# Performance work log

Hardware: AMD Instinct MI355X
Metric: run time of the kernel (lower is better)

## Reference

```python
import jax, jax.numpy as jnp
import numpy as np

N_NODES = 10000
NEG_SLOPE = 0.2
EPS = 1e-16


def gat_layer(x, W, a_src, a_dst, bias, src, dst):
    # x: [N, Fin], W: [Fin, Fout], a_src/a_dst: [Fout], bias: [Fout]
    h = x @ W                                  # [N, Fout]
    al_s = h @ a_src                           # [N]
    al_d = h @ a_dst                           # [N]
    e = jax.nn.leaky_relu(al_s[src] + al_d[dst], NEG_SLOPE)   # [E]
    # segment softmax over edges grouped by destination node
    m = jax.ops.segment_max(e, dst, num_segments=N_NODES)     # [N]
    ex = jnp.exp(e - m[dst])
    s = jax.ops.segment_sum(ex, dst, num_segments=N_NODES)    # [N]
    alpha = ex / (s[dst] + EPS)                                # [E]
    out = jax.ops.segment_sum(h[src] * alpha[:, None], dst, num_segments=N_NODES)
    return out + bias


def add_self_loops(edge_index):
    loop = jnp.arange(N_NODES, dtype=edge_index.dtype)
    return jnp.concatenate([edge_index, jnp.stack([loop, loop])], axis=1)


def setup_inputs() -> dict:
    key = jax.random.key(0)
    ks = jax.random.split(key, 12)
    F_in, F_hid, F_out = 256, 256, 256
    x = jax.random.normal(ks[0], (N_NODES, F_in), dtype=jnp.float32)
    pos_edge_index = jax.random.randint(ks[1], (2, 320000), 0, N_NODES)
    edge_index = jax.random.randint(ks[2], (2, 100000), 0, N_NODES)
    sc = lambda f: 1.0 / np.sqrt(f)
    Win_W = jax.random.normal(ks[3], (F_in, F_in), dtype=jnp.float32) * sc(F_in)
    Win_b = jnp.zeros((F_in,), dtype=jnp.float32)
    W1 = jax.random.normal(ks[4], (F_in, F_hid), dtype=jnp.float32) * sc(F_in)
    a1_src = jax.random.normal(ks[5], (F_hid,), dtype=jnp.float32) * sc(F_hid)
    a1_dst = jax.random.normal(ks[6], (F_hid,), dtype=jnp.float32) * sc(F_hid)
    b1 = jnp.zeros((F_hid,), dtype=jnp.float32)
    W2 = jax.random.normal(ks[7], (F_hid, F_out), dtype=jnp.float32) * sc(F_hid)
    a2_src = jax.random.normal(ks[8], (F_out,), dtype=jnp.float32) * sc(F_out)
    a2_dst = jax.random.normal(ks[9], (F_out,), dtype=jnp.float32) * sc(F_out)
    b2 = jnp.zeros((F_out,), dtype=jnp.float32)
    return {
        "x": x, "pos_edge_index": pos_edge_index, "edge_index": edge_index,
        "Win_W": Win_W, "Win_b": Win_b,
        "W1": W1, "a1_src": a1_src, "a1_dst": a1_dst, "b1": b1,
        "W2": W2, "a2_src": a2_src, "a2_dst": a2_dst, "b2": b2,
    }


def reference(x, pos_edge_index, edge_index, Win_W, Win_b,
              W1, a1_src, a1_dst, b1, W2, a2_src, a2_dst, b2):
    ei = add_self_loops(pos_edge_index)
    src, dst = ei[0], ei[1]
    h = x @ Win_W + Win_b                       # input_weighting Linear
    h = gat_layer(h, W1, a1_src, a1_dst, b1, src, dst)
    h = gat_layer(h, W2, a2_src, a2_dst, b2, src, dst)
    logits = jnp.sum(h[edge_index[0]] * h[edge_index[1]], axis=-1)
    return logits
```

## Files before the change

### kernel.cpp

```cpp
#include <hip/hip_runtime.h>
#include <math.h>

#define FDIM 256
#define NEG_SLOPE 0.2f

typedef _Float16 half4v __attribute__((ext_vector_type(4)));
typedef _Float16 half8v __attribute__((ext_vector_type(8)));
typedef float f32x4 __attribute__((ext_vector_type(4)));


__global__ void build_phase1(const int* __restrict__ pos_ei,
                             int* __restrict__ cnt,
                             const float* __restrict__ W0, const float* __restrict__ W1,
                             const float* __restrict__ W2,
                             _Float16* __restrict__ Wt_hi, _Float16* __restrict__ Wt_lo,
                             int E_pos, int E_tot, int nbE) {
    int b = blockIdx.x;
    int tid = threadIdx.x;
    if (b < nbE) {
        int e = b * 256 + tid;
        if (e < E_tot) {
            int d = (e < E_pos) ? pos_ei[E_pos + e] : (e - E_pos);
            atomicAdd(&cnt[d], 1);
        }
    } else {
        int idx = b - nbE;
        int n = idx & 255, mat = idx >> 8;
        const float* W = (mat == 0) ? W0 : (mat == 1) ? W1 : W2;
        int k = tid;
        float v = W[k * FDIM + n];
        _Float16 hi = (_Float16)v;
        _Float16 lo = (_Float16)(v - (float)hi);
        size_t o = (size_t)mat * FDIM * FDIM + (size_t)n * FDIM + k;
        Wt_hi[o] = hi;
        Wt_lo[o] = lo;
    }
}


__global__ __launch_bounds__(1024) void scan10k(const int* __restrict__ cnt,
                                                int* __restrict__ row_ptr,
                                                int* __restrict__ fill, int N) {
    const int CH = 10;
    __shared__ int sums[1024];
    int tid = threadIdx.x;
    int base = tid * CH;
    int vals[CH];
    int s = 0;
#pragma unroll
    for (int i = 0; i < CH; ++i) {
        int idx = base + i;
        int v = (idx < N) ? cnt[idx] : 0;
        vals[i] = s;
        s += v;
    }
    sums[tid] = s;
    __syncthreads();
    for (int off = 1; off < 1024; off <<= 1) {
        int v = (tid >= off) ? sums[tid - off] : 0;
        __syncthreads();
        sums[tid] += v;
        __syncthreads();
    }
    int toff = (tid == 0) ? 0 : sums[tid - 1];
#pragma unroll
    for (int i = 0; i < CH; ++i) {
        int idx = base + i;
        if (idx < N) {
            int rp = toff + vals[i];
            row_ptr[idx] = rp;
            fill[idx] = rp;
        }
    }
    if (tid == 0) row_ptr[N] = sums[1023];
}


__global__ void scatter_edges(const int* __restrict__ pos_ei, int* __restrict__ fill,
                              int* __restrict__ srcs, int E_pos, int E_tot) {
    int e = blockIdx.x * blockDim.x + threadIdx.x;
    if (e < E_tot) {
        int s, d;
        if (e < E_pos) { s = pos_ei[e]; d = pos_ei[E_pos + e]; }
        else           { s = e - E_pos; d = s; }
        int pos = atomicAdd(&fill[d], 1);
        srcs[pos] = s;
    }
}


template <int MODE>
__global__ __launch_bounds__(256) void gemm_mfma(
        const float* __restrict__ A32,
        const _Float16* __restrict__ A_hi, const _Float16* __restrict__ A_lo,
        const _Float16* __restrict__ Bt_hi, const _Float16* __restrict__ Bt_lo,
        const float* __restrict__ bias,
        const float* __restrict__ a_src, const float* __restrict__ a_dst,
        float* __restrict__ al_s, float* __restrict__ al_d,
        _Float16* __restrict__ C_hi, _Float16* __restrict__ C_lo,
        int M) {
    __shared__ _Float16 As_hi[64][72];
    __shared__ _Float16 As_lo[64][72];
    __shared__ _Float16 Bs_hi[64][72];
    __shared__ _Float16 Bs_lo[64][72];
    int tid = threadIdx.x;
    int lane = tid & 63, w = tid >> 6;
    int wm = w >> 1, wn = w & 1;
    int quad = lane >> 4, l16 = lane & 15;
    int mBase = blockIdx.x * 64, nBase = blockIdx.y * 64;
    f32x4 acc[2][2] = {};

    for (int k0 = 0; k0 < FDIM; k0 += 64) {
        __syncthreads();
        if (MODE == 0) {
#pragma unroll
            for (int i = 0; i < 4; ++i) {
                int f = tid + i * 256;
                int m = f >> 4, kc = (f & 15) << 2;
                int row = mBase + m;
                float4 a = make_float4(0.f, 0.f, 0.f, 0.f);
                if (row < M) a = *(const float4*)(A32 + (size_t)row * FDIM + k0 + kc);
                _Float16 hx = (_Float16)a.x, hy = (_Float16)a.y;
                _Float16 hz = (_Float16)a.z, hw = (_Float16)a.w;
                half4v hi = {hx, hy, hz, hw};
                half4v lo = {(_Float16)(a.x - (float)hx), (_Float16)(a.y - (float)hy),
                             (_Float16)(a.z - (float)hz), (_Float16)(a.w - (float)hw)};
                *(half4v*)&As_hi[m][kc] = hi;
                *(half4v*)&As_lo[m][kc] = lo;
            }
        } else {
#pragma unroll
            for (int i = 0; i < 2; ++i) {
                int g = tid + i * 256;
                int m = g >> 3, gk = (g & 7) << 3;
                int row = mBase + m;
                half8v hi, lo;
                if (row < M) {
                    size_t off = (size_t)row * FDIM + k0 + gk;
                    hi = *(const half8v*)(A_hi + off);
                    lo = *(const half8v*)(A_lo + off);
                } else {
                    _Float16 z = (_Float16)0.f;
                    hi = (half8v){z, z, z, z, z, z, z, z};
                    lo = hi;
                }
                *(half8v*)&As_hi[m][gk] = hi;
                *(half8v*)&As_lo[m][gk] = lo;
            }
        }
#pragma unroll
        for (int i = 0; i < 2; ++i) {
            int g = tid + i * 256;
            int n = g >> 3, gk = (g & 7) << 3;
            size_t off = (size_t)(nBase + n) * FDIM + k0 + gk;
            *(half8v*)&Bs_hi[n][gk] = *(const half8v*)(Bt_hi + off);
            *(half8v*)&Bs_lo[n][gk] = *(const half8v*)(Bt_lo + off);
        }
        __syncthreads();
#pragma unroll
        for (int ks = 0; ks < 2; ++ks) {
            int kcol = ks * 32 + quad * 8;
            half8v aHi[2], aLo[2], bHi[2], bLo[2];
#pragma unroll
            for (int mt = 0; mt < 2; ++mt) {
                int r = wm * 32 + mt * 16 + l16;
                aHi[mt] = *(const half8v*)&As_hi[r][kcol];
                aLo[mt] = *(const half8v*)&As_lo[r][kcol];
            }
#pragma unroll
            for (int nt = 0; nt < 2; ++nt) {
                int c = wn * 32 + nt * 16 + l16;
                bHi[nt] = *(const half8v*)&Bs_hi[c][kcol];
                bLo[nt] = *(const half8v*)&Bs_lo[c][kcol];
            }
#pragma unroll
            for (int mt = 0; mt < 2; ++mt)
#pragma unroll
                for (int nt = 0; nt < 2; ++nt) {
                    acc[mt][nt] = __builtin_amdgcn_mfma_f32_16x16x32_f16(
                        aHi[mt], bHi[nt], acc[mt][nt], 0, 0, 0);
                    acc[mt][nt] = __builtin_amdgcn_mfma_f32_16x16x32_f16(
                        aHi[mt], bLo[nt], acc[mt][nt], 0, 0, 0);
                    acc[mt][nt] = __builtin_amdgcn_mfma_f32_16x16x32_f16(
                        aLo[mt], bHi[nt], acc[mt][nt], 0, 0, 0);
                }
        }
    }

    int col0 = nBase + wn * 32 + l16;
    int col1 = col0 + 16;
    if (MODE == 0) {
        float b0 = bias[col0], b1v = bias[col1];
#pragma unroll
        for (int mt = 0; mt < 2; ++mt) {
#pragma unroll
            for (int r = 0; r < 4; ++r) {
                int row = mBase + wm * 32 + mt * 16 + quad * 4 + r;
                if (row >= M) continue;
                float o0 = acc[mt][0][r] + b0;
                float o1 = acc[mt][1][r] + b1v;
                _Float16 h0 = (_Float16)o0, h1 = (_Float16)o1;
                size_t p0 = (size_t)row * FDIM + col0;
                size_t p1 = (size_t)row * FDIM + col1;
                C_hi[p0] = h0;              C_hi[p1] = h1;
                C_lo[p0] = (_Float16)(o0 - (float)h0);
                C_lo[p1] = (_Float16)(o1 - (float)h1);
            }
        }
    } else {
        float as0 = a_src[col0], as1 = a_src[col1];
        float ad0 = a_dst[col0], ad1 = a_dst[col1];
#pragma unroll
        for (int mt = 0; mt < 2; ++mt) {
#pragma unroll
            for (int r = 0; r < 4; ++r) {
                int row = mBase + wm * 32 + mt * 16 + quad * 4 + r;
                if (row < M) {
                    C_hi[(size_t)row * FDIM + col0] = (_Float16)acc[mt][0][r];
                    C_hi[(size_t)row * FDIM + col1] = (_Float16)acc[mt][1][r];
                }
                float ps = acc[mt][0][r] * as0 + acc[mt][1][r] * as1;
                float pd = acc[mt][0][r] * ad0 + acc[mt][1][r] * ad1;
#pragma unroll
                for (int off = 8; off; off >>= 1) {
                    ps += __shfl_xor(ps, off);
                    pd += __shfl_xor(pd, off);
                }
                if (l16 == 0 && row < M) {
                    atomicAdd(&al_s[row], ps);
                    atomicAdd(&al_d[row], pd);
                }
            }
        }
    }
}


__global__ __launch_bounds__(256) void softagg(
        const _Float16* __restrict__ t, const float* __restrict__ al_s,
        const float* __restrict__ al_d, const int* __restrict__ row_ptr,
        const int* __restrict__ srcs, const float* __restrict__ bias,
        _Float16* __restrict__ out_hi, _Float16* __restrict__ out_lo,
        float* __restrict__ out32, int N) {
    int wave = threadIdx.x >> 6, lane = threadIdx.x & 63;
    int node = blockIdx.x * 4 + wave;
    if (node >= N) return;
    int beg = row_ptr[node], end = row_ptr[node + 1];
    int deg = end - beg;
    float ad = al_d[node];
    const _Float16* tb = t + (size_t)lane * 4;
    float4 acc = make_float4(0.f, 0.f, 0.f, 0.f);
    float ssum = 0.f;

    if (deg <= 256) {
        float e[4];
        int sj[4];
#pragma unroll
        for (int c = 0; c < 4; ++c) {
            e[c] = -INFINITY;
            sj[c] = 0;
            int j = beg + c * 64 + lane;
            if (j < end) {
                int s = srcs[j];
                sj[c] = s;
                float ee = al_s[s] + ad;
                e[c] = (ee > 0.f) ? ee : NEG_SLOPE * ee;
            }
        }
        float m = fmaxf(fmaxf(e[0], e[1]), fmaxf(e[2], e[3]));
#pragma unroll
        for (int o = 32; o; o >>= 1) m = fmaxf(m, __shfl_xor(m, o));
        float ex[4];
#pragma unroll
        for (int c = 0; c < 4; ++c) {
            ex[c] = (e[c] == -INFINITY) ? 0.f : __expf(e[c] - m);
            ssum += ex[c];
        }
#pragma unroll
        for (int c = 0; c < 4; ++c) {
            int jc = beg + c * 64;
            if (jc >= end) break;
            int cnt = min(64, end - jc);
            int jj = 0;
            for (; jj + 4 <= cnt; jj += 4) {
                float a0 = __shfl(ex[c], jj + 0), a1 = __shfl(ex[c], jj + 1);
                float a2 = __shfl(ex[c], jj + 2), a3 = __shfl(ex[c], jj + 3);
                int r0 = __shfl(sj[c], jj + 0), r1 = __shfl(sj[c], jj + 1);
                int r2 = __shfl(sj[c], jj + 2), r3 = __shfl(sj[c], jj + 3);
                half4v v0 = *(const half4v*)(tb + (size_t)r0 * FDIM);
                half4v v1 = *(const half4v*)(tb + (size_t)r1 * FDIM);
                half4v v2 = *(const half4v*)(tb + (size_t)r2 * FDIM);
                half4v v3 = *(const half4v*)(tb + (size_t)r3 * FDIM);
                acc.x = fmaf(a0, (float)v0.x, acc.x); acc.y = fmaf(a0, (float)v0.y, acc.y);
                acc.z = fmaf(a0, (float)v0.z, acc.z); acc.w = fmaf(a0, (float)v0.w, acc.w);
                acc.x = fmaf(a1, (float)v1.x, acc.x); acc.y = fmaf(a1, (float)v1.y, acc.y);
                acc.z = fmaf(a1, (float)v1.z, acc.z); acc.w = fmaf(a1, (float)v1.w, acc.w);
                acc.x = fmaf(a2, (float)v2.x, acc.x); acc.y = fmaf(a2, (float)v2.y, acc.y);
                acc.z = fmaf(a2, (float)v2.z, acc.z); acc.w = fmaf(a2, (float)v2.w, acc.w);
                acc.x = fmaf(a3, (float)v3.x, acc.x); acc.y = fmaf(a3, (float)v3.y, acc.y);
                acc.z = fmaf(a3, (float)v3.z, acc.z); acc.w = fmaf(a3, (float)v3.w, acc.w);
            }
            for (; jj < cnt; ++jj) {
                float a = __shfl(ex[c], jj);
                int r = __shfl(sj[c], jj);
                half4v v = *(const half4v*)(tb + (size_t)r * FDIM);
                acc.x = fmaf(a, (float)v.x, acc.x); acc.y = fmaf(a, (float)v.y, acc.y);
                acc.z = fmaf(a, (float)v.z, acc.z); acc.w = fmaf(a, (float)v.w, acc.w);
            }
        }
    } else {
        float m = -INFINITY;
        for (int j = beg + lane; j < end; j += 64) {
            float ee = al_s[srcs[j]] + ad;
            ee = (ee > 0.f) ? ee : NEG_SLOPE * ee;
            m = fmaxf(m, ee);
        }
#pragma unroll
        for (int o = 32; o; o >>= 1) m = fmaxf(m, __shfl_xor(m, o));
        for (int jc = beg; jc < end; jc += 64) {
            int j = jc + lane;
            float ex = 0.f;
            int sr = 0;
            if (j < end) {
                sr = srcs[j];
                float ee = al_s[sr] + ad;
                ee = (ee > 0.f) ? ee : NEG_SLOPE * ee;
                ex = __expf(ee - m);
                ssum += ex;
            }
            int cnt = min(64, end - jc);
            for (int jj = 0; jj < cnt; ++jj) {
                float a = __shfl(ex, jj);
                int r = __shfl(sr, jj);
                half4v v = *(const half4v*)(tb + (size_t)r * FDIM);
                acc.x = fmaf(a, (float)v.x, acc.x); acc.y = fmaf(a, (float)v.y, acc.y);
                acc.z = fmaf(a, (float)v.z, acc.z); acc.w = fmaf(a, (float)v.w, acc.w);
            }
        }
    }

#pragma unroll
    for (int o = 32; o; o >>= 1) ssum += __shfl_xor(ssum, o);
    float inv = 1.f / (ssum + 1e-16f);
    float4 bv = ((const float4*)bias)[lane];
    float ox = fmaf(acc.x, inv, bv.x);
    float oy = fmaf(acc.y, inv, bv.y);
    float oz = fmaf(acc.z, inv, bv.z);
    float ow = fmaf(acc.w, inv, bv.w);
    if (out32) {
        ((float4*)out32)[node * 64 + lane] = make_float4(ox, oy, oz, ow);
    } else {
        _Float16 hx = (_Float16)ox, hy = (_Float16)oy;
        _Float16 hz = (_Float16)oz, hw = (_Float16)ow;
        half4v hi = {hx, hy, hz, hw};
        half4v lo = {(_Float16)(ox - (float)hx), (_Float16)(oy - (float)hy),
                     (_Float16)(oz - (float)hz), (_Float16)(ow - (float)hw)};
        *(half4v*)(out_hi + (size_t)node * FDIM + lane * 4) = hi;
        *(half4v*)(out_lo + (size_t)node * FDIM + lane * 4) = lo;
    }
}


__global__ __launch_bounds__(256) void edge_dot(const float* __restrict__ h,
                                                const int* __restrict__ ei,
                                                float* __restrict__ out, int EQ) {
    int w = threadIdx.x >> 6, lane = threadIdx.x & 63;
    int e = blockIdx.x * 4 + w;
    if (e >= EQ) return;
    int u = ei[e], v = ei[EQ + e];
    const float4* hu = (const float4*)(h + (size_t)u * FDIM);
    const float4* hv = (const float4*)(h + (size_t)v * FDIM);
    float4 a = hu[lane], b = hv[lane];
    float s = a.x * b.x + a.y * b.y + a.z * b.z + a.w * b.w;
#pragma unroll
    for (int o = 32; o; o >>= 1) s += __shfl_down(s, o);
    if (lane == 0) out[e] = s;
}


extern "C" void kernel_launch(void* const* d_in, const int* in_sizes, int n_in,
                              void* d_out, int out_size, void* d_ws, size_t ws_size,
                              hipStream_t stream) {
    const float* x       = (const float*)d_in[0];
    const int*   pos_ei  = (const int*)d_in[1];
    const int*   q_ei    = (const int*)d_in[2];
    const float* Win_W   = (const float*)d_in[3];
    const float* Win_b   = (const float*)d_in[4];
    const float* W1      = (const float*)d_in[5];
    const float* a1_src  = (const float*)d_in[6];
    const float* a1_dst  = (const float*)d_in[7];
    const float* b1      = (const float*)d_in[8];
    const float* W2      = (const float*)d_in[9];
    const float* a2_src  = (const float*)d_in[10];
    const float* a2_dst  = (const float*)d_in[11];
    const float* b2      = (const float*)d_in[12];
    float* logits = (float*)d_out;

    const int N = in_sizes[0] / FDIM;
    const int E_pos = in_sizes[1] / 2;
    const int EQ = in_sizes[2] / 2;
    const int E_tot = E_pos + N;
    const size_t WMAT = (size_t)FDIM * FDIM;
    const size_t NF = (size_t)N * FDIM;

    _Float16* Wt_hi = (_Float16*)d_ws;
    _Float16* Wt_lo = Wt_hi + 3 * WMAT;
    _Float16* h0_hi = Wt_lo + 3 * WMAT;
    _Float16* h0_lo = h0_hi + NF;
    _Float16* t_h   = h0_lo + NF;
    float* h32   = (float*)(t_h + NF);
    float* al_s1 = h32 + NF;
    float* al_d1 = al_s1 + N;
    float* al_s2 = al_d1 + N;
    float* al_d2 = al_s2 + N;
    int* cnt     = (int*)(al_d2 + N);
    int* row_ptr = cnt + N;
    int* fill    = row_ptr + (N + 1);
    int* srcs    = fill + N;

    hipMemsetAsync(al_s1, 0, (size_t)(4 * N) * sizeof(float) + (size_t)N * sizeof(int), stream);

    int nbE = (E_tot + 255) / 256;

    build_phase1<<<nbE + 768, 256, 0, stream>>>(pos_ei, cnt, Win_W, W1, W2,
                                                Wt_hi, Wt_lo, E_pos, E_tot, nbE);
    scan10k<<<1, 1024, 0, stream>>>(cnt, row_ptr, fill, N);
    scatter_edges<<<nbE, 256, 0, stream>>>(pos_ei, fill, srcs, E_pos, E_tot);

    dim3 ggrid((N + 63) / 64, FDIM / 64);
    int nblk4 = (N + 3) / 4;

    gemm_mfma<0><<<ggrid, 256, 0, stream>>>(x, nullptr, nullptr, Wt_hi, Wt_lo, Win_b,
                                            nullptr, nullptr, nullptr, nullptr,
                                            h0_hi, h0_lo, N);

    gemm_mfma<1><<<ggrid, 256, 0, stream>>>(nullptr, h0_hi, h0_lo,
                                            Wt_hi + WMAT, Wt_lo + WMAT, nullptr,
                                            a1_src, a1_dst, al_s1, al_d1,
                                            t_h, nullptr, N);
    softagg<<<nblk4, 256, 0, stream>>>(t_h, al_s1, al_d1, row_ptr, srcs, b1,
                                       h0_hi, h0_lo, nullptr, N);

    gemm_mfma<1><<<ggrid, 256, 0, stream>>>(nullptr, h0_hi, h0_lo,
                                            Wt_hi + 2 * WMAT, Wt_lo + 2 * WMAT, nullptr,
                                            a2_src, a2_dst, al_s2, al_d2,
                                            t_h, nullptr, N);
    softagg<<<nblk4, 256, 0, stream>>>(t_h, al_s2, al_d2, row_ptr, srcs, b2,
                                       nullptr, nullptr, h32, N);

    edge_dot<<<(EQ + 3) / 4, 256, 0, stream>>>(h32, q_ei, logits, EQ);
}
```

Before: 238.0 us.

## Fold CSR scan and edge scatter into the GEMM launches as extra blocks

Removes the standalone scan and scatter kernels. The prefix scan now runs as one extra block appended to the first GEMM launch, rebuilt as a 256-thread scan over 40-element chunks. The edge scatter runs as extra blocks appended to the second GEMM launch. This cuts two kernel launches and lets the CSR build overlap with the GEMMs, at the cost of a slower single-block scan and a more complex GEMM kernel with a flattened 1D grid.

```diff
diff --git a/kernel.cpp b/kernel.cpp
--- a/kernel.cpp
+++ b/kernel.cpp
@@ -38,57 +38,6 @@
 }
 
 
-__global__ __launch_bounds__(1024) void scan10k(const int* __restrict__ cnt,
-                                                int* __restrict__ row_ptr,
-                                                int* __restrict__ fill, int N) {
-    const int CH = 10;
-    __shared__ int sums[1024];
-    int tid = threadIdx.x;
-    int base = tid * CH;
-    int vals[CH];
-    int s = 0;
-#pragma unroll
-    for (int i = 0; i < CH; ++i) {
-        int idx = base + i;
-        int v = (idx < N) ? cnt[idx] : 0;
-        vals[i] = s;
-        s += v;
-    }
-    sums[tid] = s;
-    __syncthreads();
-    for (int off = 1; off < 1024; off <<= 1) {
-        int v = (tid >= off) ? sums[tid - off] : 0;
-        __syncthreads();
-        sums[tid] += v;
-        __syncthreads();
-    }
-    int toff = (tid == 0) ? 0 : sums[tid - 1];
-#pragma unroll
-    for (int i = 0; i < CH; ++i) {
-        int idx = base + i;
-        if (idx < N) {
-            int rp = toff + vals[i];
-            row_ptr[idx] = rp;
-            fill[idx] = rp;
-        }
-    }
-    if (tid == 0) row_ptr[N] = sums[1023];
-}
-
-
-__global__ void scatter_edges(const int* __restrict__ pos_ei, int* __restrict__ fill,
-                              int* __restrict__ srcs, int E_pos, int E_tot) {
-    int e = blockIdx.x * blockDim.x + threadIdx.x;
-    if (e < E_tot) {
-        int s, d;
-        if (e < E_pos) { s = pos_ei[e]; d = pos_ei[E_pos + e]; }
-        else           { s = e - E_pos; d = s; }
-        int pos = atomicAdd(&fill[d], 1);
-        srcs[pos] = s;
-    }
-}
-
-
 template <int MODE>
 __global__ __launch_bounds__(256) void gemm_mfma(
         const float* __restrict__ A32,
@@ -98,16 +47,65 @@
         const float* __restrict__ a_src, const float* __restrict__ a_dst,
         float* __restrict__ al_s, float* __restrict__ al_d,
         _Float16* __restrict__ C_hi, _Float16* __restrict__ C_lo,
-        int M) {
+        int M, int nbGemm, int mblk,
+        const int* __restrict__ pos_ei, int* __restrict__ cnt_or_fill,
+        int* __restrict__ row_ptr, int* __restrict__ fill_or_srcs,
+        int E_pos, int E_tot, int N) {
     __shared__ _Float16 As_hi[64][72];
     __shared__ _Float16 As_lo[64][72];
     __shared__ _Float16 Bs_hi[64][72];
     __shared__ _Float16 Bs_lo[64][72];
+    int b = blockIdx.x;
     int tid = threadIdx.x;
+
+    if (b >= nbGemm) {
+        if (MODE == 0) {
+            int* sums = (int*)&As_hi[0][0];
+            const int CH = 40;
+            const int* cnt = cnt_or_fill;
+            int base = tid * CH;
+            int s = 0;
+            for (int i = 0; i < CH; ++i) {
+                int idx = base + i;
+                s += (idx < N) ? cnt[idx] : 0;
+            }
+            sums[tid] = s;
+            __syncthreads();
+            for (int off = 1; off < 256; off <<= 1) {
+                int v = (tid >= off) ? sums[tid - off] : 0;
+                __syncthreads();
+                sums[tid] += v;
+                __syncthreads();
+            }
+            int run = (tid == 0) ? 0 : sums[tid - 1];
+            for (int i = 0; i < CH; ++i) {
+                int idx = base + i;
+                if (idx < N) {
+                    int v = cnt[idx];
+                    row_ptr[idx] = run;
+                    fill_or_srcs[idx] = run;
+                    run += v;
+                }
+            }
+            if (tid == 255) row_ptr[N] = sums[255];
+        } else {
+            int e = (b - nbGemm) * 256 + tid;
+            if (e < E_tot) {
+                int s, d;
+                if (e < E_pos) { s = pos_ei[e]; d = pos_ei[E_pos + e]; }
+                else           { s = e - E_pos; d = s; }
+                int pos = atomicAdd(&cnt_or_fill[d], 1);
+                fill_or_srcs[pos] = s;
+            }
+        }
+        return;
+    }
+
     int lane = tid & 63, w = tid >> 6;
     int wm = w >> 1, wn = w & 1;
     int quad = lane >> 4, l16 = lane & 15;
-    int mBase = blockIdx.x * 64, nBase = blockIdx.y * 64;
+    int bx = b % mblk, by = b / mblk;
+    int mBase = bx * 64, nBase = by * 64;
     f32x4 acc[2][2] = {};
 
     for (int k0 = 0; k0 < FDIM; k0 += 64) {
@@ -421,30 +419,34 @@
     hipMemsetAsync(al_s1, 0, (size_t)(4 * N) * sizeof(float) + (size_t)N * sizeof(int), stream);
 
     int nbE = (E_tot + 255) / 256;
+    int mblk = (N + 63) / 64;
+    int nbGemm = mblk * (FDIM / 64);
+    int nblk4 = (N + 3) / 4;
 
     build_phase1<<<nbE + 768, 256, 0, stream>>>(pos_ei, cnt, Win_W, W1, W2,
                                                 Wt_hi, Wt_lo, E_pos, E_tot, nbE);
-    scan10k<<<1, 1024, 0, stream>>>(cnt, row_ptr, fill, N);
-    scatter_edges<<<nbE, 256, 0, stream>>>(pos_ei, fill, srcs, E_pos, E_tot);
-
-    dim3 ggrid((N + 63) / 64, FDIM / 64);
-    int nblk4 = (N + 3) / 4;
-
-    gemm_mfma<0><<<ggrid, 256, 0, stream>>>(x, nullptr, nullptr, Wt_hi, Wt_lo, Win_b,
-                                            nullptr, nullptr, nullptr, nullptr,
-                                            h0_hi, h0_lo, N);
-
-    gemm_mfma<1><<<ggrid, 256, 0, stream>>>(nullptr, h0_hi, h0_lo,
-                                            Wt_hi + WMAT, Wt_lo + WMAT, nullptr,
-                                            a1_src, a1_dst, al_s1, al_d1,
-                                            t_h, nullptr, N);
+
+    gemm_mfma<0><<<nbGemm + 1, 256, 0, stream>>>(
+        x, nullptr, nullptr, Wt_hi, Wt_lo, Win_b,
+        nullptr, nullptr, nullptr, nullptr, h0_hi, h0_lo,
+        N, nbGemm, mblk,
+        pos_ei, cnt, row_ptr, fill, E_pos, E_tot, N);
+
+    gemm_mfma<1><<<nbGemm + nbE, 256, 0, stream>>>(
+        nullptr, h0_hi, h0_lo, Wt_hi + WMAT, Wt_lo + WMAT, nullptr,
+        a1_src, a1_dst, al_s1, al_d1, t_h, nullptr,
+        N, nbGemm, mblk,
+        pos_ei, fill, nullptr, srcs, E_pos, E_tot, N);
+
     softagg<<<nblk4, 256, 0, stream>>>(t_h, al_s1, al_d1, row_ptr, srcs, b1,
                                        h0_hi, h0_lo, nullptr, N);
 
-    gemm_mfma<1><<<ggrid, 256, 0, stream>>>(nullptr, h0_hi, h0_lo,
-                                            Wt_hi + 2 * WMAT, Wt_lo + 2 * WMAT, nullptr,
-                                            a2_src, a2_dst, al_s2, al_d2,
-                                            t_h, nullptr, N);
+    gemm_mfma<1><<<nbGemm, 256, 0, stream>>>(
+        nullptr, h0_hi, h0_lo, Wt_hi + 2 * WMAT, Wt_lo + 2 * WMAT, nullptr,
+        a2_src, a2_dst, al_s2, al_d2, t_h, nullptr,
+        N, nbGemm, mblk,
+        nullptr, nullptr, nullptr, nullptr, 0, 0, N);
+
     softagg<<<nblk4, 256, 0, stream>>>(t_h, al_s2, al_d2, row_ptr, srcs, b2,
                                        nullptr, nullptr, h32, N);
 
```

Measured after the change: 238.8 us. About the same (+0.3%).
